# Kernel optimization log

Hardware: AMD Instinct MI355X
Metric: run time of the kernel (lower is better)

## Reference

```python
import jax, jax.numpy as jnp
import numpy as np

B, S = 512, 2048
E_DIM, P_DIM, C_DIM, H_DIM = 64, 32, 64, 64
NEG = jnp.float32(-2**32 + 1)  # padding value used by the torch module


def setup_inputs() -> dict:
    key = jax.random.key(0)
    ks = jax.random.split(key, 9)
    return {
        "seq_items": jax.random.normal(ks[0], (B, S, E_DIM), dtype=jnp.float32),
        "seq_pos": jax.random.normal(ks[1], (B, S, P_DIM), dtype=jnp.float32),
        "target_item": jax.random.normal(ks[2], (B, C_DIM), dtype=jnp.float32),
        "Wp": jax.random.normal(ks[3], (P_DIM, H_DIM), dtype=jnp.float32) * (2.0 / (P_DIM + H_DIM)) ** 0.5,
        "We": jax.random.normal(ks[4], (E_DIM, H_DIM), dtype=jnp.float32) * (2.0 / (E_DIM + H_DIM)) ** 0.5,
        "Wc": jax.random.normal(ks[5], (C_DIM, H_DIM), dtype=jnp.float32) * (2.0 / (C_DIM + H_DIM)) ** 0.5,
        "b": jnp.zeros((H_DIM,), dtype=jnp.float32),
        "z": jnp.ones((H_DIM,), dtype=jnp.float32),
        "seq_len": jax.random.randint(ks[6], (B,), 0, S, dtype=jnp.int32),
    }


def reference(seq_items, seq_pos, target_item, Wp, We, Wc, b, z, seq_len):
    # Projections: [B,h] and [B,S,h]
    out_c = target_item @ Wc                      # [B, h]
    out_e = jnp.einsum("bse,eh->bsh", seq_items, We)
    out_p = jnp.einsum("bsp,ph->bsh", seq_pos, Wp)
    # Additive attention score: [B, S]
    a = jnp.sum(jnp.tanh(out_c[:, None, :] + out_p + out_e + b) * z, axis=-1)
    # seq_len mask
    mask = jnp.arange(seq_items.shape[1])[None, :] < seq_len[:, None]  # [B, S]
    score = jax.nn.softmax(jnp.where(mask, a, NEG), axis=1)            # [B, S]
    # u = score @ e -> [B, 1, e_dim]  (intended unsqueeze(1) matmul)
    u = jnp.einsum("bs,bse->be", score, seq_items)[:, None, :]
    # r = sum of masked raw scores -> [B, 1]
    r = jnp.sum(jnp.where(mask, a, 0.0), axis=1, keepdims=True)
    return (u, r)
```

## Files before the change

kernel.cpp:

```cpp
#include <hip/hip_runtime.h>
#include <hip/hip_bf16.h>
#include <math.h>

#define B_ 512
#define S_ 2048
#define E_DIM 64
#define P_DIM 32
#define H_DIM 64
#define CB_STRIDE 68

typedef short s16x8 __attribute__((ext_vector_type(8)));
typedef int i32x4 __attribute__((ext_vector_type(4)));
typedef float f32x4 __attribute__((ext_vector_type(4)));

__device__ __forceinline__ float wave_reduce_sum(float v) {
#pragma unroll
  for (int m = 32; m >= 1; m >>= 1) v += __shfl_xor(v, m, 64);
  return v;
}

__device__ __forceinline__ float wave_reduce_max(float v) {
#pragma unroll
  for (int m = 32; m >= 1; m >>= 1) v = fmaxf(v, __shfl_xor(v, m, 64));
  return v;
}

__device__ __forceinline__ float tanh_fast(float x) {
  float e = __expf(2.0f * x);
  return 1.0f - 2.0f * __builtin_amdgcn_rcpf(e + 1.0f);
}

__device__ __forceinline__ short bf16b(float x) {
  union { float f; unsigned u; } a;
  a.f = x;
  unsigned r = (a.u + 0x7FFFu + ((a.u >> 16) & 1u)) >> 16;
  return (short)r;
}

__device__ __forceinline__ int cvt_pk2(float a, float b) {
  union { __hip_bfloat162 v; int i; } u;
  u.v = __float22bfloat162_rn(make_float2(a, b));
  return u.i;
}

__device__ __forceinline__ s16x8 cvt8(float4 lo, float4 hi) {
  i32x4 r;
  r[0] = cvt_pk2(lo.x, lo.y);
  r[1] = cvt_pk2(lo.z, lo.w);
  r[2] = cvt_pk2(hi.x, hi.y);
  r[3] = cvt_pk2(hi.z, hi.w);
  return __builtin_bit_cast(s16x8, r);
}

__global__ __launch_bounds__(256) void precompute_kernel(
    const float* __restrict__ target_item, const float* __restrict__ Wp,
    const float* __restrict__ We, const float* __restrict__ Wc,
    const float* __restrict__ bias, s16x8* __restrict__ frags,
    float* __restrict__ c_all) {
  const int tid = threadIdx.x;
  const int l = tid & 63;
  if (blockIdx.x == 0) {
    const int w = tid >> 6;
    const int cc = l & 15;
    const int q = l >> 4;
#pragma unroll
    for (int i = 0; i < 3; ++i) {
      const int f = w * 3 + i;
      const int kstep = f >> 2;
      const int nt = f & 3;
      const float* __restrict__ src =
          (kstep < 2)
              ? (We + (size_t)(kstep * 32 + q * 8) * H_DIM + nt * 16 + cc)
              : (Wp + (size_t)(q * 8) * H_DIM + nt * 16 + cc);
      s16x8 v;
#pragma unroll
      for (int j = 0; j < 8; ++j) v[j] = bf16b(src[(size_t)j * H_DIM]);
      frags[f * 64 + l] = v;
    }
  } else {
    const int b = (blockIdx.x - 1) * 4 + (tid >> 6);
    const int h = l;
    const float* __restrict__ tg = target_item + b * E_DIM;
    float c = bias[h];
#pragma unroll
    for (int e = 0; e < 64; ++e) c = fmaf(tg[e], Wc[e * H_DIM + h], c);
    c_all[b * H_DIM + h] = c;
  }
}

__global__ __launch_bounds__(256) void scores_mfma_kernel(
    const float* __restrict__ seq_items, const float* __restrict__ seq_pos,
    const float* __restrict__ z, const int* __restrict__ seq_len,
    const s16x8* __restrict__ frags, const float* __restrict__ c_all,
    float* __restrict__ chunk_buf) {
  const int blk = blockIdx.x;
  const int b = blk >> 4;
  const int s0 = (blk & 15) << 7;
  const int L = seq_len[b];
  const bool uni = (L == 0);
  if (!uni && s0 >= L) return;

  __shared__ float s_a[128];
  __shared__ float s_w[128];
  __shared__ __align__(16) float s_pc[4 * 64];
  __shared__ float redm[4], reds[4], redr[4];

  const int tid = threadIdx.x;
  const int l = tid & 63;
  const int w = tid >> 6;
  const int cc = l & 15;
  const int q = l >> 4;

  s16x8 bfr[12];
#pragma unroll
  for (int f = 0; f < 12; ++f) bfr[f] = frags[f * 64 + l];

  float ch[4], zh[4];
#pragma unroll
  for (int nt = 0; nt < 4; ++nt) {
    const int h = nt * 16 + cc;
    ch[nt] = c_all[b * H_DIM + h];
    zh[nt] = z[h];
  }

  const float* __restrict__ itemsB = seq_items + (size_t)b * S_ * E_DIM;
  const float* __restrict__ posB = seq_pos + (size_t)b * S_ * P_DIM;

  float4 xi[2][4];
  float4 xp[2][2];
#pragma unroll
  for (int mt = 0; mt < 2; ++mt) {
    const int s = s0 + w * 32 + mt * 16 + cc;
    const float* __restrict__ pi = itemsB + (size_t)s * E_DIM + q * 8;
    xi[mt][0] = ((const float4*)pi)[0];
    xi[mt][1] = ((const float4*)pi)[1];
    xi[mt][2] = ((const float4*)(pi + 32))[0];
    xi[mt][3] = ((const float4*)(pi + 32))[1];
    const float* __restrict__ pp = posB + (size_t)s * P_DIM + q * 8;
    xp[mt][0] = ((const float4*)pp)[0];
    xp[mt][1] = ((const float4*)pp)[1];
  }

  s16x8 afr[2][3];
#pragma unroll
  for (int mt = 0; mt < 2; ++mt) {
    afr[mt][0] = cvt8(xi[mt][0], xi[mt][1]);
    afr[mt][1] = cvt8(xi[mt][2], xi[mt][3]);
    afr[mt][2] = cvt8(xp[mt][0], xp[mt][1]);
  }

#pragma unroll
  for (int mt = 0; mt < 2; ++mt) {
    f32x4 acc[4] = {};
#pragma unroll
    for (int kk = 0; kk < 2; ++kk) {
#pragma unroll
      for (int nt = 0; nt < 4; ++nt)
        acc[nt] = __builtin_amdgcn_mfma_f32_16x16x32_bf16(
            afr[mt][kk], bfr[kk * 4 + nt], acc[nt], 0, 0, 0);
    }
#pragma unroll
    for (int nt = 0; nt < 4; ++nt)
      acc[nt] = __builtin_amdgcn_mfma_f32_16x16x32_bf16(
          afr[mt][2], bfr[8 + nt], acc[nt], 0, 0, 0);

    float asum[4];
#pragma unroll
    for (int r = 0; r < 4; ++r) {
      float t = tanh_fast(acc[0][r] + ch[0]) * zh[0];
      t += tanh_fast(acc[1][r] + ch[1]) * zh[1];
      t += tanh_fast(acc[2][r] + ch[2]) * zh[2];
      t += tanh_fast(acc[3][r] + ch[3]) * zh[3];
      asum[r] = t;
    }
#pragma unroll
    for (int r = 0; r < 4; ++r) {
#pragma unroll
      for (int m = 8; m >= 1; m >>= 1) asum[r] += __shfl_xor(asum[r], m, 64);
    }
    if (cc == 0) {
#pragma unroll
      for (int r = 0; r < 4; ++r) s_a[w * 32 + mt * 16 + q * 4 + r] = asum[r];
    }
  }

  __syncthreads();
  const int row = tid & 127;
  const int srow = s0 + row;
  const bool valid = uni || (srow < L);
  const float araw = s_a[row];
  const float ae = uni ? 0.0f : araw;
  float mp = wave_reduce_max(valid ? ae : -INFINITY);
  if (l == 0) redm[w] = mp;
  __syncthreads();
  const float mc = fmaxf(fmaxf(redm[0], redm[1]), fmaxf(redm[2], redm[3]));
  const float wgt = valid ? __expf(ae - mc) : 0.0f;
  if (tid < 128) s_w[row] = wgt;
  const float scp = wave_reduce_sum(wgt);
  const float rap = wave_reduce_sum(valid ? ae : 0.0f);
  if (l == 0) { reds[w] = scp; redr[w] = rap; }
  __syncthreads();

  {
    const int e4 = l & 15;
    const int rr = l >> 4;
    const float4* __restrict__ ip4 =
        (const float4*)(itemsB + (size_t)(s0 + w * 32) * E_DIM);
    float4 a4 = make_float4(0.f, 0.f, 0.f, 0.f);
#pragma unroll
    for (int i = 0; i < 8; ++i) {
      const int rloc = rr + i * 4;
      const float g = s_w[w * 32 + rloc];
      const float4 x = ip4[rloc * 16 + e4];
      a4.x = fmaf(g, x.x, a4.x);
      a4.y = fmaf(g, x.y, a4.y);
      a4.z = fmaf(g, x.z, a4.z);
      a4.w = fmaf(g, x.w, a4.w);
    }
#pragma unroll
    for (int m = 16; m <= 32; m <<= 1) {
      a4.x += __shfl_xor(a4.x, m, 64);
      a4.y += __shfl_xor(a4.y, m, 64);
      a4.z += __shfl_xor(a4.z, m, 64);
      a4.w += __shfl_xor(a4.w, m, 64);
    }
    if (rr == 0) *(float4*)&s_pc[w * 64 + e4 * 4] = a4;
  }
  __syncthreads();

  float* __restrict__ cb = chunk_buf + (size_t)blk * CB_STRIDE;
  if (tid < 64) {
    cb[tid] = s_pc[tid] + s_pc[64 + tid] + s_pc[128 + tid] + s_pc[192 + tid];
  } else if (tid == 64) {
    cb[64] = mc;
  } else if (tid == 65) {
    cb[65] = reds[0] + reds[1];
  } else if (tid == 66) {
    cb[66] = redr[0] + redr[1];
  }
}

__global__ __launch_bounds__(64) void combine_kernel(
    const float* __restrict__ chunk_buf, const int* __restrict__ seq_len,
    float* __restrict__ out) {
  const int b = blockIdx.x;
  const int t = threadIdx.x;
  const int L = seq_len[b];
  const int nc = (L == 0) ? 16 : ((L + 127) >> 7);
  const float* __restrict__ cb = chunk_buf + (size_t)b * 16 * CB_STRIDE;

  float m = -INFINITY;
  for (int c = 0; c < nc; ++c) m = fmaxf(m, cb[c * CB_STRIDE + 64]);
  float u = 0.0f, den = 0.0f, r = 0.0f;
  for (int c = 0; c < nc; ++c) {
    const float e = __expf(cb[c * CB_STRIDE + 64] - m);
    u = fmaf(e, cb[c * CB_STRIDE + t], u);
    den = fmaf(e, cb[c * CB_STRIDE + 65], den);
    r += cb[c * CB_STRIDE + 66];
  }
  out[b * E_DIM + t] = u / den;
  if (t == 0) out[B_ * E_DIM + b] = r;
}

extern "C" void kernel_launch(void* const* d_in, const int* in_sizes, int n_in,
                              void* d_out, int out_size, void* d_ws, size_t ws_size,
                              hipStream_t stream) {
  const float* seq_items = (const float*)d_in[0];
  const float* seq_pos = (const float*)d_in[1];
  const float* target_item = (const float*)d_in[2];
  const float* Wp = (const float*)d_in[3];
  const float* We = (const float*)d_in[4];
  const float* Wc = (const float*)d_in[5];
  const float* bias = (const float*)d_in[6];
  const float* z = (const float*)d_in[7];
  const int* seq_len = (const int*)d_in[8];
  float* out = (float*)d_out;

  float* chunk_buf = (float*)d_ws;
  float* c_all = (float*)d_ws + (size_t)B_ * 16 * CB_STRIDE;
  s16x8* frags =
      (s16x8*)((float*)d_ws + (size_t)B_ * 16 * CB_STRIDE + B_ * H_DIM);

  precompute_kernel<<<129, 256, 0, stream>>>(target_item, Wp, We, Wc, bias,
                                             frags, c_all);
  scores_mfma_kernel<<<B_ * 16, 256, 0, stream>>>(seq_items, seq_pos, z,
                                                  seq_len, frags, c_all,
                                                  chunk_buf);
  combine_kernel<<<B_, 64, 0, stream>>>(chunk_buf, seq_len, out);
}
```

Measured before the change: 439.6 us.

## Fuse combine into scores kernel via per-batch atomic counter and per-wave partials

Removes the separate combine kernel launch: each wave now writes its own partial softmax state (max, sum, weighted item sum, raw sum) and bumps a per-batch atomic counter, and the last arriving wave performs the final cross-chunk merge. Block-level __syncthreads and shared-memory reductions are replaced with wave-local reductions, and waves whose rows are all beyond seq_len skip the loads and MFMA work. The cost is four times as many partial records, a longer serial merge loop in the last wave, and threadfence/atomic traffic.

Result: slower. 1.494 ms (+239.9%).

```diff
diff --git a/kernel.cpp b/kernel.cpp
--- a/kernel.cpp
+++ b/kernel.cpp
@@ -56,10 +56,12 @@
     const float* __restrict__ target_item, const float* __restrict__ Wp,
     const float* __restrict__ We, const float* __restrict__ Wc,
     const float* __restrict__ bias, s16x8* __restrict__ frags,
-    float* __restrict__ c_all) {
+    float* __restrict__ c_all, unsigned* __restrict__ cnt) {
   const int tid = threadIdx.x;
   const int l = tid & 63;
   if (blockIdx.x == 0) {
+    cnt[tid] = 0u;
+    cnt[256 + tid] = 0u;
     const int w = tid >> 6;
     const int cc = l & 15;
     const int q = l >> 4;
@@ -92,7 +94,8 @@
     const float* __restrict__ seq_items, const float* __restrict__ seq_pos,
     const float* __restrict__ z, const int* __restrict__ seq_len,
     const s16x8* __restrict__ frags, const float* __restrict__ c_all,
-    float* __restrict__ chunk_buf) {
+    float* __restrict__ chunk_buf, unsigned* __restrict__ cnt,
+    float* __restrict__ out) {
   const int blk = blockIdx.x;
   const int b = blk >> 4;
   const int s0 = (blk & 15) << 7;
@@ -100,118 +103,126 @@
   const bool uni = (L == 0);
   if (!uni && s0 >= L) return;
 
-  __shared__ float s_a[128];
   __shared__ float s_w[128];
-  __shared__ __align__(16) float s_pc[4 * 64];
-  __shared__ float redm[4], reds[4], redr[4];
 
   const int tid = threadIdx.x;
   const int l = tid & 63;
   const int w = tid >> 6;
   const int cc = l & 15;
   const int q = l >> 4;
-
-  s16x8 bfr[12];
-#pragma unroll
-  for (int f = 0; f < 12; ++f) bfr[f] = frags[f * 64 + l];
-
-  float ch[4], zh[4];
-#pragma unroll
-  for (int nt = 0; nt < 4; ++nt) {
-    const int h = nt * 16 + cc;
-    ch[nt] = c_all[b * H_DIM + h];
-    zh[nt] = z[h];
-  }
-
-  const float* __restrict__ itemsB = seq_items + (size_t)b * S_ * E_DIM;
-  const float* __restrict__ posB = seq_pos + (size_t)b * S_ * P_DIM;
-
-  float4 xi[2][4];
-  float4 xp[2][2];
-#pragma unroll
-  for (int mt = 0; mt < 2; ++mt) {
-    const int s = s0 + w * 32 + mt * 16 + cc;
-    const float* __restrict__ pi = itemsB + (size_t)s * E_DIM + q * 8;
-    xi[mt][0] = ((const float4*)pi)[0];
-    xi[mt][1] = ((const float4*)pi)[1];
-    xi[mt][2] = ((const float4*)(pi + 32))[0];
-    xi[mt][3] = ((const float4*)(pi + 32))[1];
-    const float* __restrict__ pp = posB + (size_t)s * P_DIM + q * 8;
-    xp[mt][0] = ((const float4*)pp)[0];
-    xp[mt][1] = ((const float4*)pp)[1];
-  }
-
-  s16x8 afr[2][3];
-#pragma unroll
-  for (int mt = 0; mt < 2; ++mt) {
-    afr[mt][0] = cvt8(xi[mt][0], xi[mt][1]);
-    afr[mt][1] = cvt8(xi[mt][2], xi[mt][3]);
-    afr[mt][2] = cvt8(xp[mt][0], xp[mt][1]);
-  }
-
-#pragma unroll
-  for (int mt = 0; mt < 2; ++mt) {
-    f32x4 acc[4] = {};
-#pragma unroll
-    for (int kk = 0; kk < 2; ++kk) {
+  const int rowbase = s0 + w * 32;
+  const int cw = ((blk & 15) << 2) | w;
+  float* __restrict__ cb = chunk_buf + ((size_t)b * 64 + cw) * CB_STRIDE;
+
+  const bool waveActive = uni || (rowbase < L);
+  if (waveActive) {
+    const float* __restrict__ itemsB = seq_items + (size_t)b * S_ * E_DIM;
+    const float* __restrict__ posB = seq_pos + (size_t)b * S_ * P_DIM;
+
+    float4 xi[2][4];
+    float4 xp[2][2];
+#pragma unroll
+    for (int mt = 0; mt < 2; ++mt) {
+      const int s = rowbase + mt * 16 + cc;
+      const float* __restrict__ pi = itemsB + (size_t)s * E_DIM + q * 8;
+      xi[mt][0] = ((const float4*)pi)[0];
+      xi[mt][1] = ((const float4*)pi)[1];
+      xi[mt][2] = ((const float4*)(pi + 32))[0];
+      xi[mt][3] = ((const float4*)(pi + 32))[1];
+      const float* __restrict__ pp = posB + (size_t)s * P_DIM + q * 8;
+      xp[mt][0] = ((const float4*)pp)[0];
+      xp[mt][1] = ((const float4*)pp)[1];
+    }
+
+    s16x8 bfr[12];
+#pragma unroll
+    for (int f = 0; f < 12; ++f) bfr[f] = frags[f * 64 + l];
+    float ch[4], zh[4];
+#pragma unroll
+    for (int nt = 0; nt < 4; ++nt) {
+      const int h = nt * 16 + cc;
+      ch[nt] = c_all[b * H_DIM + h];
+      zh[nt] = z[h];
+    }
+
+    s16x8 afr[2][3];
+#pragma unroll
+    for (int mt = 0; mt < 2; ++mt) {
+      afr[mt][0] = cvt8(xi[mt][0], xi[mt][1]);
+      afr[mt][1] = cvt8(xi[mt][2], xi[mt][3]);
+      afr[mt][2] = cvt8(xp[mt][0], xp[mt][1]);
+    }
+
+    float asum[2][4];
+#pragma unroll
+    for (int mt = 0; mt < 2; ++mt) {
+      f32x4 acc[4] = {};
+#pragma unroll
+      for (int kk = 0; kk < 2; ++kk) {
+#pragma unroll
+        for (int nt = 0; nt < 4; ++nt)
+          acc[nt] = __builtin_amdgcn_mfma_f32_16x16x32_bf16(
+              afr[mt][kk], bfr[kk * 4 + nt], acc[nt], 0, 0, 0);
+      }
 #pragma unroll
       for (int nt = 0; nt < 4; ++nt)
         acc[nt] = __builtin_amdgcn_mfma_f32_16x16x32_bf16(
-            afr[mt][kk], bfr[kk * 4 + nt], acc[nt], 0, 0, 0);
-    }
-#pragma unroll
-    for (int nt = 0; nt < 4; ++nt)
-      acc[nt] = __builtin_amdgcn_mfma_f32_16x16x32_bf16(
-          afr[mt][2], bfr[8 + nt], acc[nt], 0, 0, 0);
-
-    float asum[4];
-#pragma unroll
-    for (int r = 0; r < 4; ++r) {
-      float t = tanh_fast(acc[0][r] + ch[0]) * zh[0];
-      t += tanh_fast(acc[1][r] + ch[1]) * zh[1];
-      t += tanh_fast(acc[2][r] + ch[2]) * zh[2];
-      t += tanh_fast(acc[3][r] + ch[3]) * zh[3];
-      asum[r] = t;
-    }
-#pragma unroll
-    for (int r = 0; r < 4; ++r) {
-#pragma unroll
-      for (int m = 8; m >= 1; m >>= 1) asum[r] += __shfl_xor(asum[r], m, 64);
-    }
+            afr[mt][2], bfr[8 + nt], acc[nt], 0, 0, 0);
+
+#pragma unroll
+      for (int r = 0; r < 4; ++r) {
+        float t = tanh_fast(acc[0][r] + ch[0]) * zh[0];
+        t += tanh_fast(acc[1][r] + ch[1]) * zh[1];
+        t += tanh_fast(acc[2][r] + ch[2]) * zh[2];
+        t += tanh_fast(acc[3][r] + ch[3]) * zh[3];
+#pragma unroll
+        for (int m = 8; m >= 1; m >>= 1) t += __shfl_xor(t, m, 64);
+        asum[mt][r] = t;
+      }
+    }
+
+    float mx = -INFINITY, racc = 0.0f;
+    float ae[2][4];
+#pragma unroll
+    for (int mt = 0; mt < 2; ++mt) {
+#pragma unroll
+      for (int r = 0; r < 4; ++r) {
+        const int srow = rowbase + mt * 16 + q * 4 + r;
+        const bool valid = uni || (srow < L);
+        ae[mt][r] = uni ? 0.0f : (valid ? asum[mt][r] : -INFINITY);
+        racc += (!uni && valid) ? asum[mt][r] : 0.0f;
+        mx = fmaxf(mx, ae[mt][r]);
+      }
+    }
+    mx = wave_reduce_max(mx);
+    float wgt[2][4];
+    float wsum = 0.0f;
+#pragma unroll
+    for (int mt = 0; mt < 2; ++mt) {
+#pragma unroll
+      for (int r = 0; r < 4; ++r) {
+        wgt[mt][r] = __expf(ae[mt][r] - mx);
+        wsum += wgt[mt][r];
+      }
+    }
+    const float scv = wave_reduce_sum(wsum) * 0.0625f;
+    const float rav = wave_reduce_sum(racc) * 0.0625f;
+
     if (cc == 0) {
 #pragma unroll
-      for (int r = 0; r < 4; ++r) s_a[w * 32 + mt * 16 + q * 4 + r] = asum[r];
-    }
-  }
-
-  __syncthreads();
-  const int row = tid & 127;
-  const int srow = s0 + row;
-  const bool valid = uni || (srow < L);
-  const float araw = s_a[row];
-  const float ae = uni ? 0.0f : araw;
-  float mp = wave_reduce_max(valid ? ae : -INFINITY);
-  if (l == 0) redm[w] = mp;
-  __syncthreads();
-  const float mc = fmaxf(fmaxf(redm[0], redm[1]), fmaxf(redm[2], redm[3]));
-  const float wgt = valid ? __expf(ae - mc) : 0.0f;
-  if (tid < 128) s_w[row] = wgt;
-  const float scp = wave_reduce_sum(wgt);
-  const float rap = wave_reduce_sum(valid ? ae : 0.0f);
-  if (l == 0) { reds[w] = scp; redr[w] = rap; }
-  __syncthreads();
-
-  {
-    const int e4 = l & 15;
-    const int rr = l >> 4;
-    const float4* __restrict__ ip4 =
-        (const float4*)(itemsB + (size_t)(s0 + w * 32) * E_DIM);
+      for (int mt = 0; mt < 2; ++mt)
+#pragma unroll
+        for (int r = 0; r < 4; ++r)
+          s_w[w * 32 + mt * 16 + q * 4 + r] = wgt[mt][r];
+    }
+
+    const float4* __restrict__ ip4 = (const float4*)itemsB;
     float4 a4 = make_float4(0.f, 0.f, 0.f, 0.f);
 #pragma unroll
     for (int i = 0; i < 8; ++i) {
-      const int rloc = rr + i * 4;
+      const int rloc = q + i * 4;
       const float g = s_w[w * 32 + rloc];
-      const float4 x = ip4[rloc * 16 + e4];
+      const float4 x = ip4[(size_t)(rowbase + rloc) * 16 + cc];
       a4.x = fmaf(g, x.x, a4.x);
       a4.y = fmaf(g, x.y, a4.y);
       a4.z = fmaf(g, x.z, a4.z);
@@ -224,42 +235,42 @@
       a4.z += __shfl_xor(a4.z, m, 64);
       a4.w += __shfl_xor(a4.w, m, 64);
     }
-    if (rr == 0) *(float4*)&s_pc[w * 64 + e4 * 4] = a4;
+    if (q == 0) *(float4*)(cb + cc * 4) = a4;
+    if (l == 16) cb[64] = mx;
+    if (l == 17) cb[65] = scv;
+    if (l == 18) cb[66] = rav;
+  } else {
+    if (l < 16) {
+      f32x4 zz = {};
+      *(f32x4*)(cb + l * 4) = zz;
+    }
+    if (l == 16) cb[64] = -INFINITY;
+    if (l == 17) cb[65] = 0.0f;
+    if (l == 18) cb[66] = 0.0f;
   }
-  __syncthreads();
-
-  float* __restrict__ cb = chunk_buf + (size_t)blk * CB_STRIDE;
-  if (tid < 64) {
-    cb[tid] = s_pc[tid] + s_pc[64 + tid] + s_pc[128 + tid] + s_pc[192 + tid];
-  } else if (tid == 64) {
-    cb[64] = mc;
-  } else if (tid == 65) {
-    cb[65] = reds[0] + reds[1];
-  } else if (tid == 66) {
-    cb[66] = redr[0] + redr[1];
+
+  __threadfence();
+  const int nch = uni ? 16 : ((L + 127) >> 7);
+  const unsigned expected = (unsigned)(nch << 2);
+  unsigned old = 0;
+  if (l == 0) old = atomicAdd(&cnt[b], 1u);
+  old = (unsigned)__shfl((int)old, 0, 64);
+  if (old == expected - 1u) {
+    __threadfence();
+    const float* __restrict__ cbb = chunk_buf + (size_t)b * 64 * CB_STRIDE;
+    float m = -INFINITY;
+    for (int c = 0; c < (int)expected; ++c)
+      m = fmaxf(m, cbb[c * CB_STRIDE + 64]);
+    float u = 0.0f, den = 0.0f, rsum = 0.0f;
+    for (int c = 0; c < (int)expected; ++c) {
+      const float e = __expf(cbb[c * CB_STRIDE + 64] - m);
+      u = fmaf(e, cbb[c * CB_STRIDE + l], u);
+      den = fmaf(e, cbb[c * CB_STRIDE + 65], den);
+      rsum += cbb[c * CB_STRIDE + 66];
+    }
+    out[b * E_DIM + l] = u / den;
+    if (l == 0) out[B_ * E_DIM + b] = rsum;
   }
-}
-
-__global__ __launch_bounds__(64) void combine_kernel(
-    const float* __restrict__ chunk_buf, const int* __restrict__ seq_len,
-    float* __restrict__ out) {
-  const int b = blockIdx.x;
-  const int t = threadIdx.x;
-  const int L = seq_len[b];
-  const int nc = (L == 0) ? 16 : ((L + 127) >> 7);
-  const float* __restrict__ cb = chunk_buf + (size_t)b * 16 * CB_STRIDE;
-
-  float m = -INFINITY;
-  for (int c = 0; c < nc; ++c) m = fmaxf(m, cb[c * CB_STRIDE + 64]);
-  float u = 0.0f, den = 0.0f, r = 0.0f;
-  for (int c = 0; c < nc; ++c) {
-    const float e = __expf(cb[c * CB_STRIDE + 64] - m);
-    u = fmaf(e, cb[c * CB_STRIDE + t], u);
-    den = fmaf(e, cb[c * CB_STRIDE + 65], den);
-    r += cb[c * CB_STRIDE + 66];
-  }
-  out[b * E_DIM + t] = u / den;
-  if (t == 0) out[B_ * E_DIM + b] = r;
 }
 
 extern "C" void kernel_launch(void* const* d_in, const int* in_sizes, int n_in,
@@ -277,14 +288,14 @@
   float* out = (float*)d_out;
 
   float* chunk_buf = (float*)d_ws;
-  float* c_all = (float*)d_ws + (size_t)B_ * 16 * CB_STRIDE;
-  s16x8* frags =
-      (s16x8*)((float*)d_ws + (size_t)B_ * 16 * CB_STRIDE + B_ * H_DIM);
+  float* c_all = chunk_buf + (size_t)B_ * 64 * CB_STRIDE;
+  float* frags_f = c_all + (size_t)B_ * H_DIM;
+  s16x8* frags = (s16x8*)frags_f;
+  unsigned* cnt = (unsigned*)(frags_f + 12 * 64 * 4);
 
   precompute_kernel<<<129, 256, 0, stream>>>(target_item, Wp, We, Wc, bias,
-                                             frags, c_all);
+                                             frags, c_all, cnt);
   scores_mfma_kernel<<<B_ * 16, 256, 0, stream>>>(seq_items, seq_pos, z,
                                                   seq_len, frags, c_all,
-                                                  chunk_buf);
-  combine_kernel<<<B_, 64, 0, stream>>>(chunk_buf, seq_len, out);
-}
+                                                  chunk_buf, cnt, out);
+}
```
